# Kernel tuning notes

Hardware: AMD Instinct MI355X
Metric: run time of the kernel (lower is better)

## Reference

```python
import jax, jax.numpy as jnp
import numpy as np

D = 1280      # emb_dim
H = 4         # n_heads
DH = D // H
FF = 256      # dim_feedforward / hidden_dim
NL = 2        # n_layers
B = 64        # number of graphs
N = 32768     # total tokens
L = 640       # max padded length (>= max graph size w.h.p.)
EPS = 1e-5


def setup_inputs() -> dict:
    key = jax.random.key(0)
    ks = jax.random.split(key, 24)
    s = 0.02
    x = jax.random.normal(ks[0], (N, D), jnp.float32)
    batch = jnp.sort(jax.random.randint(ks[1], (N,), 0, B))
    p = {
        "x": x, "batch": batch,
        # stacked per-layer transformer params (torch Linear convention: y = x @ W.T + b)
        "Wqkv": jax.random.normal(ks[2], (NL, 3 * D, D), jnp.float32) * s,
        "bqkv": jnp.zeros((NL, 3 * D), jnp.float32),
        "Wo":   jax.random.normal(ks[3], (NL, D, D), jnp.float32) * s,
        "bo":   jnp.zeros((NL, D), jnp.float32),
        "ln1w": jnp.ones((NL, D), jnp.float32),
        "ln1b": jnp.zeros((NL, D), jnp.float32),
        "W1":   jax.random.normal(ks[4], (NL, FF, D), jnp.float32) * s,
        "b1":   jnp.zeros((NL, FF), jnp.float32),
        "W2":   jax.random.normal(ks[5], (NL, D, FF), jnp.float32) * s,
        "b2":   jnp.zeros((NL, D), jnp.float32),
        "ln2w": jnp.ones((NL, D), jnp.float32),
        "ln2b": jnp.zeros((NL, D), jnp.float32),
        # final MLP: Linear(D,FF) -> ReLU -> Linear(FF,D)
        "Wm1": jax.random.normal(ks[6], (FF, D), jnp.float32) * s,
        "bm1": jnp.zeros((FF,), jnp.float32),
        "Wm2": jax.random.normal(ks[7], (D, FF), jnp.float32) * s,
        "bm2": jnp.zeros((D,), jnp.float32),
    }
    return p


def _ln(x, w, b):
    mu = jnp.mean(x, axis=-1, keepdims=True)
    var = jnp.var(x, axis=-1, keepdims=True)
    return (x - mu) * jax.lax.rsqrt(var + EPS) * w + b


def reference(x, batch, Wqkv, bqkv, Wo, bo, ln1w, ln1b, W1, b1, W2, b2,
              ln2w, ln2b, Wm1, bm1, Wm2, bm2):
    # --- graph_to_transformer_input: scatter ragged tokens into [B, L, D] ---
    counts = jax.ops.segment_sum(jnp.ones_like(batch), batch, num_segments=B)
    offsets = jnp.concatenate([jnp.zeros((1,), counts.dtype), jnp.cumsum(counts)[:-1]])
    pos = jnp.arange(N) - offsets[batch]                 # position within each graph
    padded = jnp.zeros((B, L, D), x.dtype).at[batch, pos].set(x)
    pad_mask = jnp.arange(L)[None, :] >= counts[:, None]  # True = padding key

    h = padded
    scale = 1.0 / np.sqrt(DH)
    for l in range(NL):  # post-norm TransformerEncoderLayer, relu, dropout=eval
        qkv = h @ Wqkv[l].T + bqkv[l]
        q, k, v = jnp.split(qkv, 3, axis=-1)
        sh = lambda t: t.reshape(B, L, H, DH).transpose(0, 2, 1, 3)  # [B,H,L,DH]
        q, k, v = sh(q), sh(k), sh(v)
        scores = jnp.einsum('bhqd,bhkd->bhqk', q, k) * scale
        scores = jnp.where(pad_mask[:, None, None, :], -1e9, scores)
        attn = jax.nn.softmax(scores, axis=-1)
        o = jnp.einsum('bhqk,bhkd->bhqd', attn, v).transpose(0, 2, 1, 3).reshape(B, L, D)
        o = o @ Wo[l].T + bo[l]
        h = _ln(h + o, ln1w[l], ln1b[l])
        ff = jax.nn.relu(h @ W1[l].T + b1[l]) @ W2[l].T + b2[l]
        h = _ln(h + ff, ln2w[l], ln2b[l])

    forces = jax.nn.relu(h @ Wm1.T + bm1) @ Wm2.T + bm2   # [B, L, D]
    return forces[batch, pos]                              # gather valid tokens -> [N, D]
```

## Files before the change

kernel.cpp:

```cpp
#include <hip/hip_runtime.h>

typedef unsigned short u16;
typedef __attribute__((ext_vector_type(8))) short bf16x8;
typedef __attribute__((ext_vector_type(4))) float f32x4;

#define N_TOK 32768
#define DIM   1280
#define NH    4
#define DH    320
#define FFD   256
#define NLAYER 2
#define NB    64
#define TD    3840
#define KVD   2560

#define GLD16(gp, lp) __builtin_amdgcn_global_load_lds( \
    (const __attribute__((address_space(1))) unsigned int*)(const void*)(gp), \
    (__attribute__((address_space(3))) unsigned int*)(void*)(lp), 16, 0, 0)

__device__ __forceinline__ float b2f(u16 v) {
    union { unsigned u; float f; } c; c.u = ((unsigned)v) << 16; return c.f;
}
__device__ __forceinline__ u16 f2b(float f) {
    union { float f; unsigned u; } c; c.f = f;
    unsigned r = c.u + 0x7fffu + ((c.u >> 16) & 1u);
    return (u16)(r >> 16);
}

__global__ __launch_bounds__(256) void k_f32_to_bf16(
    const float* __restrict__ in, u16* __restrict__ out, long n)
{
    long i = ((long)blockIdx.x * 256 + threadIdx.x) * 4;
    if (i >= n) return;
    float4 v = *(const float4*)&in[i];
    ushort4 o; o.x = f2b(v.x); o.y = f2b(v.y); o.z = f2b(v.z); o.w = f2b(v.w);
    *(ushort4*)&out[i] = o;
}

#define E0 9830400L
#define E1 13107200L
#define E2 13762560L
#define E3 14417920L
#define E4 14745600L
#define E5 15073280L
__global__ __launch_bounds__(256) void k_conv_weights(
    const float* __restrict__ Wqkv, const float* __restrict__ Wo,
    const float* __restrict__ W1,   const float* __restrict__ W2,
    const float* __restrict__ Wm1,  const float* __restrict__ Wm2,
    u16* __restrict__ d0, u16* __restrict__ d1, u16* __restrict__ d2,
    u16* __restrict__ d3, u16* __restrict__ d4, u16* __restrict__ d5)
{
    long i = ((long)blockIdx.x * 256 + threadIdx.x) * 4;
    if (i >= E5) return;
    const float* src; u16* dst; long off;
    if      (i < E0) { src = Wqkv; dst = d0; off = i; }
    else if (i < E1) { src = Wo;   dst = d1; off = i - E0; }
    else if (i < E2) { src = W1;   dst = d2; off = i - E1; }
    else if (i < E3) { src = W2;   dst = d3; off = i - E2; }
    else if (i < E4) { src = Wm1;  dst = d4; off = i - E3; }
    else             { src = Wm2;  dst = d5; off = i - E4; }
    float4 v = *(const float4*)&src[off];
    ushort4 o; o.x = f2b(v.x); o.y = f2b(v.y); o.z = f2b(v.z); o.w = f2b(v.w);
    *(ushort4*)&dst[off] = o;
}

__global__ void k_offsets(const int* __restrict__ batch, int* __restrict__ offs) {
    int b = threadIdx.x;
    if (b > NB) return;
    int lo = 0, hi = N_TOK;
    while (lo < hi) {
        int mid = (lo + hi) >> 1;
        if (batch[mid] < b) lo = mid + 1; else hi = mid;
    }
    offs[b] = lo;
}

__global__ __launch_bounds__(256) void k_gemm_mfma(
    const u16* __restrict__ A, int lda,
    const u16* __restrict__ W,
    const float* __restrict__ bias,
    void* __restrict__ Cv, int ldc,
    int K, int relu, int store_f32)
{
    __shared__ u16 Asm[128 * 64];
    __shared__ u16 Bsm[128 * 64];
    const int t    = threadIdx.x;
    const int lane = t & 63;
    const int w    = t >> 6;
    const int wr   = w >> 1, wc = w & 1;
    const long mBase = (long)blockIdx.y * 128;
    const long nBase = (long)blockIdx.x * 128;
    const int srow = lane >> 3;
    const int scol = (lane & 7) * 8;

    f32x4 acc[4][4];
    #pragma unroll
    for (int m = 0; m < 4; ++m)
        #pragma unroll
        for (int n = 0; n < 4; ++n) acc[m][n] = (f32x4){0.f, 0.f, 0.f, 0.f};

    for (int k0 = 0; k0 < K; k0 += 64) {
        __syncthreads();
        #pragma unroll
        for (int i = 0; i < 4; ++i) {
            const int c = w * 4 + i;
            const u16* ga = &A[(mBase + c * 8 + srow) * (long)lda + k0 + scol];
            const u16* gb = &W[(nBase + c * 8 + srow) * (long)K   + k0 + scol];
            GLD16(ga, &Asm[c * 512]);
            GLD16(gb, &Bsm[c * 512]);
        }
        __syncthreads();
        #pragma unroll
        for (int kk = 0; kk < 2; ++kk) {
            const int kc = kk * 32 + (lane >> 4) * 8;
            bf16x8 af[4], bfr[4];
            #pragma unroll
            for (int m = 0; m < 4; ++m)
                af[m] = *(const bf16x8*)&Asm[(wr * 64 + m * 16 + (lane & 15)) * 64 + kc];
            #pragma unroll
            for (int n = 0; n < 4; ++n)
                bfr[n] = *(const bf16x8*)&Bsm[(wc * 64 + n * 16 + (lane & 15)) * 64 + kc];
            #pragma unroll
            for (int m = 0; m < 4; ++m)
                #pragma unroll
                for (int n = 0; n < 4; ++n)
                    acc[m][n] = __builtin_amdgcn_mfma_f32_16x16x32_bf16(
                        af[m], bfr[n], acc[m][n], 0, 0, 0);
        }
    }

    const int ccol  = lane & 15;
    const int crow0 = (lane >> 4) * 4;
    #pragma unroll
    for (int m = 0; m < 4; ++m) {
        #pragma unroll
        for (int n = 0; n < 4; ++n) {
            const long col = nBase + wc * 64 + n * 16 + ccol;
            const float bv = bias[col];
            #pragma unroll
            for (int r = 0; r < 4; ++r) {
                const long row = mBase + wr * 64 + m * 16 + crow0 + r;
                float v = acc[m][n][r] + bv;
                if (relu) v = fmaxf(v, 0.f);
                if (store_f32) ((float*)Cv)[row * (long)ldc + col] = v;
                else           ((u16*)Cv)[row * (long)ldc + col] = f2b(v);
            }
        }
    }
}

__global__ __launch_bounds__(256) void k_gemm_qkv(
    const u16* __restrict__ A,
    const u16* __restrict__ W,
    const float* __restrict__ bias,
    u16* __restrict__ qd, u16* __restrict__ kvd)
{
    __shared__ u16 Asm[128 * 64];
    __shared__ u16 Bsm[128 * 64];
    const int t    = threadIdx.x;
    const int lane = t & 63;
    const int w    = t >> 6;
    const int wr   = w >> 1, wc = w & 1;
    const long mBase = (long)blockIdx.y * 128;
    const long nBase = (long)blockIdx.x * 128;
    const int srow = lane >> 3;
    const int scol = (lane & 7) * 8;

    f32x4 acc[4][4];
    #pragma unroll
    for (int m = 0; m < 4; ++m)
        #pragma unroll
        for (int n = 0; n < 4; ++n) acc[m][n] = (f32x4){0.f, 0.f, 0.f, 0.f};

    for (int k0 = 0; k0 < DIM; k0 += 64) {
        __syncthreads();
        #pragma unroll
        for (int i = 0; i < 4; ++i) {
            const int c = w * 4 + i;
            const u16* ga = &A[(mBase + c * 8 + srow) * (long)DIM + k0 + scol];
            const u16* gb = &W[(nBase + c * 8 + srow) * (long)DIM + k0 + scol];
            GLD16(ga, &Asm[c * 512]);
            GLD16(gb, &Bsm[c * 512]);
        }
        __syncthreads();
        #pragma unroll
        for (int kk = 0; kk < 2; ++kk) {
            const int kc = kk * 32 + (lane >> 4) * 8;
            bf16x8 af[4], bfr[4];
            #pragma unroll
            for (int m = 0; m < 4; ++m)
                af[m] = *(const bf16x8*)&Asm[(wr * 64 + m * 16 + (lane & 15)) * 64 + kc];
            #pragma unroll
            for (int n = 0; n < 4; ++n)
                bfr[n] = *(const bf16x8*)&Bsm[(wc * 64 + n * 16 + (lane & 15)) * 64 + kc];
            #pragma unroll
            for (int m = 0; m < 4; ++m)
                #pragma unroll
                for (int n = 0; n < 4; ++n)
                    acc[m][n] = __builtin_amdgcn_mfma_f32_16x16x32_bf16(
                        af[m], bfr[n], acc[m][n], 0, 0, 0);
        }
    }

    const int ccol  = lane & 15;
    const int crow0 = (lane >> 4) * 4;
    const bool isQ = (nBase < DIM);
    #pragma unroll
    for (int m = 0; m < 4; ++m) {
        #pragma unroll
        for (int n = 0; n < 4; ++n) {
            const long col = nBase + wc * 64 + n * 16 + ccol;
            const float bv = bias[col];
            #pragma unroll
            for (int r = 0; r < 4; ++r) {
                const long row = mBase + wr * 64 + m * 16 + crow0 + r;
                float v = acc[m][n][r] + bv;
                if (isQ) qd[row * (long)DIM + col]          = f2b(v);
                else     kvd[row * (long)KVD + (col - DIM)] = f2b(v);
            }
        }
    }
}

__global__ __launch_bounds__(256) void k_ln_residual(
    const u16* __restrict__ a, const u16* __restrict__ delta,
    const float* __restrict__ w, const float* __restrict__ bb,
    u16* __restrict__ out)
{
    const int lane = threadIdx.x & 63;
    const long row = (long)blockIdx.x * 4 + (threadIdx.x >> 6);
    const long base = row * DIM + lane * 20;
    float v[20];
    float s = 0.f, s2 = 0.f;
    #pragma unroll
    for (int k = 0; k < 5; ++k) {
        uint2 ua = *(const uint2*)&a[base + k * 4];
        uint2 ud = *(const uint2*)&delta[base + k * 4];
        u16 ah[4], dh[4];
        *(uint2*)ah = ua; *(uint2*)dh = ud;
        #pragma unroll
        for (int e = 0; e < 4; ++e) {
            float xv = b2f(ah[e]) + b2f(dh[e]);
            v[k * 4 + e] = xv; s += xv; s2 += xv * xv;
        }
    }
    #pragma unroll
    for (int off = 32; off > 0; off >>= 1) {
        s  += __shfl_xor(s, off);
        s2 += __shfl_xor(s2, off);
    }
    const float mu  = s * (1.f / DIM);
    const float var = s2 * (1.f / DIM) - mu * mu;
    const float inv = rsqrtf(fmaxf(var, 0.f) + 1e-5f);
    const int cb = lane * 20;
    #pragma unroll
    for (int k = 0; k < 5; ++k) {
        float4 wv = *(const float4*)&w[cb + k * 4];
        float4 bv = *(const float4*)&bb[cb + k * 4];
        u16 oh[4];
        oh[0] = f2b((v[k * 4 + 0] - mu) * inv * wv.x + bv.x);
        oh[1] = f2b((v[k * 4 + 1] - mu) * inv * wv.y + bv.y);
        oh[2] = f2b((v[k * 4 + 2] - mu) * inv * wv.z + bv.z);
        oh[3] = f2b((v[k * 4 + 3] - mu) * inv * wv.w + bv.w);
        *(uint2*)&out[base + k * 4] = *(uint2*)oh;
    }
}

__global__ __launch_bounds__(512) void k_attn_mfma(
    u16* __restrict__ q, const u16* __restrict__ kv, const int* __restrict__ offs)
{
    __shared__ u16 KV[21760];
    __shared__ float Ssm[64 * 65];
    __shared__ u16 Plds[64 * 72];
    __shared__ float mL[64], lL[64], aL[64];

    const int lin = blockIdx.x;
    const int gLo = lin & 7;
    const int j   = lin >> 3;
    const int g   = (j / 40) * 8 + gLo;
    const int rem = j % 40;
    const int hh  = rem / 10;
    const int qt  = rem % 10;

    const int gstart = offs[g];
    const int n = offs[g + 1] - gstart;
    if (qt * 64 >= n) return;
    const int nq = min(64, n - qt * 64);
    const int t    = threadIdx.x;
    const int lane = t & 63;
    const int w    = t >> 6;
    const int qr   = w >> 1, kr = w & 1;
    const int rh   = w >> 2, fs = w & 3;
    const int l15  = lane & 15;
    const int l4   = lane >> 4;
    const float scale = 0.05590169943749474f;

    if (t < 64) { mL[t] = -1e30f; lL[t] = 0.f; }

    bf16x8 qf[10];
    {
        int qrl = qt * 64 + qr * 16 + l15;
        if (qrl >= n) qrl = n - 1;
        const u16* gq = &q[(long)(gstart + qrl) * DIM + hh * DH + l4 * 8];
        #pragma unroll
        for (int c = 0; c < 10; ++c)
            qf[c] = *(const bf16x8*)&gq[c * 32];
    }

    f32x4 oacc[2][5];
    #pragma unroll
    for (int a = 0; a < 2; ++a)
        #pragma unroll
        for (int f = 0; f < 5; ++f) oacc[a][f] = (f32x4){0.f, 0.f, 0.f, 0.f};

    const int spos = t >> 3;
    const int sfb  = (t & 7) * 40;
    const int vpp  = t & 31;
    const int vfb  = (t >> 5) * 20;

    for (int kb = 0; kb < n; kb += 64) {
        const int nk = min(64, n - kb);
        __syncthreads();

        {
            int gp = kb + spos; if (gp >= n) gp = n - 1;
            const u16* gk = &kv[(long)(gstart + gp) * KVD + hh * DH + sfb];
            uint4 c0 = *(const uint4*)(gk + 0);
            uint4 c1 = *(const uint4*)(gk + 8);
            uint4 c2 = *(const uint4*)(gk + 16);
            uint4 c3 = *(const uint4*)(gk + 24);
            uint4 c4 = *(const uint4*)(gk + 32);
            u16* dst = &KV[spos * 328 + sfb];
            *(uint4*)(dst + 0)  = c0;
            *(uint4*)(dst + 8)  = c1;
            *(uint4*)(dst + 16) = c2;
            *(uint4*)(dst + 24) = c3;
            *(uint4*)(dst + 32) = c4;
        }
        __syncthreads();

        #pragma unroll
        for (int kk = 0; kk < 2; ++kk) {
            const int colb = kr * 32 + kk * 16;
            f32x4 sacc = (f32x4){0.f, 0.f, 0.f, 0.f};
            #pragma unroll
            for (int c = 0; c < 10; ++c) {
                bf16x8 kf = *(const bf16x8*)&KV[(colb + l15) * 328 + c * 32 + l4 * 8];
                sacc = __builtin_amdgcn_mfma_f32_16x16x32_bf16(qf[c], kf, sacc, 0, 0, 0);
            }
            const int col = colb + l15;
            const int srow0 = qr * 16 + l4 * 4;
            const bool masked = (col >= nk);
            #pragma unroll
            for (int r = 0; r < 4; ++r)
                Ssm[(srow0 + r) * 65 + col] = masked ? -1e30f : sacc[r] * scale;
        }
        __syncthreads();

        {
            uint2 va4[5], vb4[5];
            {
                int p0 = kb + 2 * vpp, p1 = p0 + 1;
                if (p0 >= n) p0 = n - 1;
                if (p1 >= n) p1 = n - 1;
                const u16* g0 = &kv[(long)(gstart + p0) * KVD + DIM + hh * DH + vfb];
                const u16* g1 = &kv[(long)(gstart + p1) * KVD + DIM + hh * DH + vfb];
                #pragma unroll
                for (int i = 0; i < 5; ++i) {
                    va4[i] = *(const uint2*)(g0 + i * 4);
                    vb4[i] = *(const uint2*)(g1 + i * 4);
                }
            }

            const int r  = t >> 3;
            const int cg = (t & 7) * 8;
            float4 sa = *(const float4*)&Ssm[r * 65 + cg];
            float4 sb = *(const float4*)&Ssm[r * 65 + cg + 4];
            float mx = fmaxf(fmaxf(fmaxf(sa.x, sa.y), fmaxf(sa.z, sa.w)),
                             fmaxf(fmaxf(sb.x, sb.y), fmaxf(sb.z, sb.w)));
            mx = fmaxf(mx, __shfl_xor(mx, 1));
            mx = fmaxf(mx, __shfl_xor(mx, 2));
            mx = fmaxf(mx, __shfl_xor(mx, 4));
            const float mo = mL[r];
            const float mn = fmaxf(mo, mx);
            float p0f = __expf(sa.x - mn), p1f = __expf(sa.y - mn);
            float p2f = __expf(sa.z - mn), p3f = __expf(sa.w - mn);
            float p4f = __expf(sb.x - mn), p5f = __expf(sb.y - mn);
            float p6f = __expf(sb.z - mn), p7f = __expf(sb.w - mn);
            union { u16 h[8]; uint4 u; } pw;
            pw.h[0] = f2b(p0f); pw.h[1] = f2b(p1f); pw.h[2] = f2b(p2f); pw.h[3] = f2b(p3f);
            pw.h[4] = f2b(p4f); pw.h[5] = f2b(p5f); pw.h[6] = f2b(p6f); pw.h[7] = f2b(p7f);
            *(uint4*)&Plds[r * 72 + cg] = pw.u;
            float rs = ((p0f + p1f) + (p2f + p3f)) + ((p4f + p5f) + (p6f + p7f));
            rs += __shfl_xor(rs, 1);
            rs += __shfl_xor(rs, 2);
            rs += __shfl_xor(rs, 4);
            if ((t & 7) == 0) {
                const float al = __expf(mo - mn);
                aL[r] = al;
                lL[r] = lL[r] * al + rs;
                mL[r] = mn;
            }
            {
                const int colp = 2 * vpp;
                #pragma unroll
                for (int i = 0; i < 5; ++i) {
                    const unsigned a0 = va4[i].x, a1 = va4[i].y;
                    const unsigned b0 = vb4[i].x, b1 = vb4[i].y;
                    const int fb = vfb + i * 4;
                    *(unsigned*)&KV[(fb + 0) * 68 + colp] = (a0 & 0xffffu) | (b0 << 16);
                    *(unsigned*)&KV[(fb + 1) * 68 + colp] = (a0 >> 16) | (b0 & 0xffff0000u);
                    *(unsigned*)&KV[(fb + 2) * 68 + colp] = (a1 & 0xffffu) | (b1 << 16);
                    *(unsigned*)&KV[(fb + 3) * 68 + colp] = (a1 >> 16) | (b1 & 0xffff0000u);
                }
            }
        }
        __syncthreads();

        {
            float al[2][4];
            #pragma unroll
            for (int a = 0; a < 2; ++a)
                #pragma unroll
                for (int r = 0; r < 4; ++r)
                    al[a][r] = aL[rh * 32 + a * 16 + l4 * 4 + r];
            #pragma unroll
            for (int a = 0; a < 2; ++a)
                #pragma unroll
                for (int f = 0; f < 5; ++f)
                    #pragma unroll
                    for (int r = 0; r < 4; ++r)
                        oacc[a][f][r] *= al[a][r];
            #pragma unroll
            for (int ks = 0; ks < 2; ++ks) {
                #pragma unroll
                for (int a = 0; a < 2; ++a) {
                    bf16x8 pf = *(const bf16x8*)&Plds[(rh * 32 + a * 16 + l15) * 72 + ks * 32 + l4 * 8];
                    #pragma unroll
                    for (int f = 0; f < 5; ++f) {
                        const int fe = fs * 80 + f * 16 + l15;
                        union { bf16x8 v; uint2 u[2]; } uv;
                        uv.u[0] = *(const uint2*)&KV[fe * 68 + ks * 32 + l4 * 8];
                        uv.u[1] = *(const uint2*)&KV[fe * 68 + ks * 32 + l4 * 8 + 4];
                        oacc[a][f] = __builtin_amdgcn_mfma_f32_16x16x32_bf16(
                            pf, uv.v, oacc[a][f], 0, 0, 0);
                    }
                }
            }
        }
    }

    float invl[2][4];
    #pragma unroll
    for (int a = 0; a < 2; ++a)
        #pragma unroll
        for (int r = 0; r < 4; ++r)
            invl[a][r] = 1.f / lL[rh * 32 + a * 16 + l4 * 4 + r];
    #pragma unroll
    for (int a = 0; a < 2; ++a) {
        #pragma unroll
        for (int f = 0; f < 5; ++f) {
            #pragma unroll
            for (int r = 0; r < 4; ++r) {
                const int lrow = rh * 32 + a * 16 + l4 * 4 + r;
                if (lrow < nq) {
                    const long grow = (long)(gstart + qt * 64 + lrow);
                    q[grow * DIM + hh * DH + fs * 80 + f * 16 + l15] =
                        f2b(oacc[a][f][r] * invl[a][r]);
                }
            }
        }
    }
}

extern "C" void kernel_launch(void* const* d_in, const int* in_sizes, int n_in,
                              void* d_out, int out_size, void* d_ws, size_t ws_size,
                              hipStream_t stream) {
    const float* x     = (const float*)d_in[0];
    const int*   batch = (const int*)d_in[1];
    const float* Wqkv  = (const float*)d_in[2];
    const float* bqkv  = (const float*)d_in[3];
    const float* Wo    = (const float*)d_in[4];
    const float* bo    = (const float*)d_in[5];
    const float* ln1w  = (const float*)d_in[6];
    const float* ln1b  = (const float*)d_in[7];
    const float* W1    = (const float*)d_in[8];
    const float* b1    = (const float*)d_in[9];
    const float* W2    = (const float*)d_in[10];
    const float* b2    = (const float*)d_in[11];
    const float* ln2w  = (const float*)d_in[12];
    const float* ln2b  = (const float*)d_in[13];
    const float* Wm1   = (const float*)d_in[14];
    const float* bm1   = (const float*)d_in[15];
    const float* Wm2   = (const float*)d_in[16];
    const float* bm2   = (const float*)d_in[17];

    float* outF = (float*)d_out;
    u16*   qbuf = (u16*)d_out;

    char* ws   = (char*)d_ws;
    int*  offs = (int*)ws;
    u16*  h    = (u16*)(ws + 1024);
    u16*  kvb  = h + (size_t)N_TOK * DIM;
    u16*  tmp  = kvb;
    u16*  ff   = kvb + (size_t)N_TOK * DIM;
    u16*  wqkv_bf = kvb + (size_t)N_TOK * KVD;
    u16*  wo_bf   = wqkv_bf + (size_t)NLAYER * TD * DIM;
    u16*  w1_bf   = wo_bf   + (size_t)NLAYER * DIM * DIM;
    u16*  w2_bf   = w1_bf   + (size_t)NLAYER * FFD * DIM;
    u16*  wm1_bf  = w2_bf   + (size_t)NLAYER * DIM * FFD;
    u16*  wm2_bf  = wm1_bf  + (size_t)FFD * DIM;

    k_offsets<<<1, 128, 0, stream>>>(batch, offs);
    {
        long n = (long)N_TOK * DIM;
        k_f32_to_bf16<<<(int)(n / 1024), 256, 0, stream>>>(x, h, n);
        k_conv_weights<<<(int)(E5 / 1024), 256, 0, stream>>>(
            Wqkv, Wo, W1, W2, Wm1, Wm2,
            wqkv_bf, wo_bf, w1_bf, w2_bf, wm1_bf, wm2_bf);
    }

    dim3 blk(256);
    for (int l = 0; l < NLAYER; ++l) {
        const u16*   Wl = wqkv_bf + (size_t)l * TD * DIM;
        const float* bl = bqkv + (size_t)l * TD;
        k_gemm_qkv<<<dim3(TD / 128, N_TOK / 128), blk, 0, stream>>>(
            h, Wl, bl, qbuf, kvb);
        k_attn_mfma<<<dim3(10 * NH * NB), dim3(512), 0, stream>>>(qbuf, kvb, offs);
        k_gemm_mfma<<<dim3(DIM / 128, N_TOK / 128), blk, 0, stream>>>(
            qbuf, DIM, wo_bf + (size_t)l * DIM * DIM, bo + (size_t)l * DIM,
            tmp, DIM, DIM, 0, 0);
        k_ln_residual<<<N_TOK / 4, blk, 0, stream>>>(
            h, tmp, ln1w + (size_t)l * DIM, ln1b + (size_t)l * DIM, h);
        k_gemm_mfma<<<dim3(FFD / 128, N_TOK / 128), blk, 0, stream>>>(
            h, DIM, w1_bf + (size_t)l * FFD * DIM, b1 + (size_t)l * FFD,
            ff, FFD, DIM, 1, 0);
        k_gemm_mfma<<<dim3(DIM / 128, N_TOK / 128), blk, 0, stream>>>(
            ff, FFD, w2_bf + (size_t)l * DIM * FFD, b2 + (size_t)l * DIM,
            tmp, DIM, FFD, 0, 0);
        k_ln_residual<<<N_TOK / 4, blk, 0, stream>>>(
            h, tmp, ln2w + (size_t)l * DIM, ln2b + (size_t)l * DIM, h);
    }
    k_gemm_mfma<<<dim3(FFD / 128, N_TOK / 128), blk, 0, stream>>>(
        h, DIM, wm1_bf, bm1, ff, FFD, DIM, 1, 0);
    k_gemm_mfma<<<dim3(DIM / 128, N_TOK / 128), blk, 0, stream>>>(
        ff, FFD, wm2_bf, bm2, outF, DIM, FFD, 0, 1);
}
```

Measured before the change: 2.574 ms.

## Add 256x256-tile 8-wave QKV GEMM with ping-pong LDS pipeline

Adds a new QKV projection kernel that uses 256x256 output tiles, 512 threads and 128KB of dynamic LDS. It double-buffers K-slices loaded with global_load_lds and interleaves the loads for upcoming quadrants with MFMA phases, using explicit vmcnt waits and barriers. The goal is more operand reuse per block and better overlap of memory traffic with MFMA work than the 128x128 kernel provides. It falls back to the old kernel if the large LDS allocation cannot be set, and the larger tile lowers occupancy and adds many barriers.

New measurement: 2.934 ms. +14.0%, slower.

```diff
diff --git a/kernel.cpp b/kernel.cpp
--- a/kernel.cpp
+++ b/kernel.cpp
@@ -222,6 +222,133 @@
     }
 }
 
+__global__ __launch_bounds__(512) void k_gemm_qkv8(
+    const u16* __restrict__ A,
+    const u16* __restrict__ W,
+    const float* __restrict__ bias,
+    u16* __restrict__ qd, u16* __restrict__ kvd)
+{
+    extern __shared__ u16 dynlds[];
+    u16* Alds = dynlds;
+    u16* Blds = dynlds + 32768;
+    const int t    = threadIdx.x;
+    const int lane = t & 63;
+    const int w    = t >> 6;
+    const int wm2  = w >> 2;
+    const int wn2  = w & 3;
+    const int l15  = lane & 15;
+    const int l4   = lane >> 4;
+    const long mBase = (long)blockIdx.y * 256;
+    const long nBase = (long)blockIdx.x * 256;
+
+    f32x4 acc[2][2][4][2];
+    #pragma unroll
+    for (int a = 0; a < 2; ++a)
+        #pragma unroll
+        for (int b = 0; b < 2; ++b)
+            #pragma unroll
+            for (int c = 0; c < 4; ++c)
+                #pragma unroll
+                for (int d = 0; d < 2; ++d)
+                    acc[a][b][c][d] = (f32x4){0.f, 0.f, 0.f, 0.f};
+
+#define SA(T, H) { \
+    GLD16(&A[(mBase + (H) * 128 + (t >> 3)) * (long)DIM + (T) * 64 + (t & 7) * 8], \
+          &Alds[((T) & 1) * 16384 + (H) * 8192 + t * 8]); \
+    GLD16(&A[(mBase + (H) * 128 + 64 + (t >> 3)) * (long)DIM + (T) * 64 + (t & 7) * 8], \
+          &Alds[((T) & 1) * 16384 + (H) * 8192 + 4096 + t * 8]); }
+#define SB(T, H) { \
+    GLD16(&W[(nBase + (H) * 128 + (t >> 3)) * (long)DIM + (T) * 64 + (t & 7) * 8], \
+          &Blds[((T) & 1) * 16384 + (H) * 8192 + t * 8]); \
+    GLD16(&W[(nBase + (H) * 128 + 64 + (t >> 3)) * (long)DIM + (T) * 64 + (t & 7) * 8], \
+          &Blds[((T) & 1) * 16384 + (H) * 8192 + 4096 + t * 8]); }
+
+#define PH(T, QM, QN, WAITC, STG) { \
+    WAITC; \
+    bf16x8 afr[4][2]; bf16x8 bfr[2][2]; \
+    const int bo = ((T) & 1) * 16384; \
+    _Pragma("unroll") \
+    for (int ks = 0; ks < 2; ++ks) { \
+        _Pragma("unroll") \
+        for (int f = 0; f < 4; ++f) \
+            afr[f][ks] = *(const bf16x8*)&Alds[bo + ((QM) * 128 + wm2 * 64 + f * 16 + l15) * 64 + ks * 32 + l4 * 8]; \
+        _Pragma("unroll") \
+        for (int g = 0; g < 2; ++g) \
+            bfr[g][ks] = *(const bf16x8*)&Blds[bo + ((QN) * 128 + wn2 * 32 + g * 16 + l15) * 64 + ks * 32 + l4 * 8]; \
+    } \
+    STG; \
+    __builtin_amdgcn_s_barrier(); \
+    _Pragma("unroll") \
+    for (int ks = 0; ks < 2; ++ks) \
+        _Pragma("unroll") \
+        for (int f = 0; f < 4; ++f) \
+            _Pragma("unroll") \
+            for (int g = 0; g < 2; ++g) \
+                acc[QM][QN][f][g] = __builtin_amdgcn_mfma_f32_16x16x32_bf16( \
+                    afr[f][ks], bfr[g][ks], acc[QM][QN][f][g], 0, 0, 0); \
+    __builtin_amdgcn_s_barrier(); }
+
+#define VM4 asm volatile("s_waitcnt vmcnt(4)" ::: "memory")
+#define VM2 asm volatile("s_waitcnt vmcnt(2)" ::: "memory")
+#define VM0 asm volatile("s_waitcnt vmcnt(0)" ::: "memory")
+#define NOW
+
+    SA(0, 0); SB(0, 0); SB(0, 1); SA(0, 1);
+    SA(1, 0); SB(1, 0);
+    VM4;
+    __builtin_amdgcn_s_barrier();
+
+    const int nIter = (DIM / 64) / 2;
+    for (int it = 0; it < nIter - 1; ++it) {
+        const int t0 = it * 2, t1 = t0 + 1, t2 = t0 + 2, t3 = t0 + 3;
+        PH(t0, 0, 0, NOW, { SB(t1, 1); })
+        PH(t0, 0, 1, NOW, { SA(t1, 1); })
+        PH(t0, 1, 0, NOW, { SA(t2, 0); })
+        PH(t0, 1, 1, VM2, { SB(t2, 0); })
+        PH(t1, 0, 0, NOW, { SB(t2, 1); })
+        PH(t1, 0, 1, NOW, { SA(t2, 1); })
+        PH(t1, 1, 0, NOW, { SA(t3, 0); })
+        PH(t1, 1, 1, VM2, { SB(t3, 0); })
+    }
+    {
+        const int t0 = (nIter - 1) * 2, t1 = t0 + 1;
+        PH(t0, 0, 0, NOW, { SB(t1, 1); })
+        PH(t0, 0, 1, NOW, { SA(t1, 1); })
+        PH(t0, 1, 0, NOW, {})
+        PH(t0, 1, 1, VM0, {})
+        PH(t1, 0, 0, NOW, {})
+        PH(t1, 0, 1, NOW, {})
+        PH(t1, 1, 0, NOW, {})
+        PH(t1, 1, 1, NOW, {})
+    }
+
+    #pragma unroll
+    for (int qm = 0; qm < 2; ++qm)
+        #pragma unroll
+        for (int qn = 0; qn < 2; ++qn)
+            #pragma unroll
+            for (int f = 0; f < 4; ++f)
+                #pragma unroll
+                for (int g = 0; g < 2; ++g) {
+                    const long col = nBase + qn * 128 + wn2 * 32 + g * 16 + l15;
+                    const float bv = bias[col];
+                    #pragma unroll
+                    for (int r = 0; r < 4; ++r) {
+                        const long row = mBase + qm * 128 + wm2 * 64 + f * 16 + l4 * 4 + r;
+                        float v = acc[qm][qn][f][g][r] + bv;
+                        if (col < DIM) qd[row * (long)DIM + col] = f2b(v);
+                        else           kvd[row * (long)KVD + (col - DIM)] = f2b(v);
+                    }
+                }
+#undef SA
+#undef SB
+#undef PH
+#undef VM4
+#undef VM2
+#undef VM0
+#undef NOW
+}
+
 __global__ __launch_bounds__(256) void k_ln_residual(
     const u16* __restrict__ a, const u16* __restrict__ delta,
     const float* __restrict__ w, const float* __restrict__ bb,
@@ -299,7 +426,7 @@
 
     bf16x8 qf[10];
     {
-        int qrl = qt * 64 + qr * 16 + l15;
+        int qrl = qt * 64 + w * 0 + qr * 16 + l15;
         if (qrl >= n) qrl = n - 1;
         const u16* gq = &q[(long)(gstart + qrl) * DIM + hh * DH + l4 * 8];
         #pragma unroll
@@ -511,6 +638,11 @@
     u16*  wm1_bf  = w2_bf   + (size_t)NLAYER * DIM * FFD;
     u16*  wm2_bf  = wm1_bf  + (size_t)FFD * DIM;
 
+    const bool use8 =
+        (hipFuncSetAttribute((const void*)k_gemm_qkv8,
+                             hipFuncAttributeMaxDynamicSharedMemorySize,
+                             131072) == hipSuccess);
+
     k_offsets<<<1, 128, 0, stream>>>(batch, offs);
     {
         long n = (long)N_TOK * DIM;
@@ -524,8 +656,13 @@
     for (int l = 0; l < NLAYER; ++l) {
         const u16*   Wl = wqkv_bf + (size_t)l * TD * DIM;
         const float* bl = bqkv + (size_t)l * TD;
-        k_gemm_qkv<<<dim3(TD / 128, N_TOK / 128), blk, 0, stream>>>(
-            h, Wl, bl, qbuf, kvb);
+        if (use8) {
+            k_gemm_qkv8<<<dim3(TD / 256, N_TOK / 256), dim3(512), 131072, stream>>>(
+                h, Wl, bl, qbuf, kvb);
+        } else {
+            k_gemm_qkv<<<dim3(TD / 128, N_TOK / 128), blk, 0, stream>>>(
+                h, Wl, bl, qbuf, kvb);
+        }
         k_attn_mfma<<<dim3(10 * NH * NB), dim3(512), 0, stream>>>(qbuf, kvb, offs);
         k_gemm_mfma<<<dim3(DIM / 128, N_TOK / 128), blk, 0, stream>>>(
             qbuf, DIM, wo_bf + (size_t)l * DIM * DIM, bo + (size_t)l * DIM,
```
